# Kernel optimization log

Hardware: AMD Instinct MI355X
Metric: run time of the kernel (lower is better)

Reference implementation:

```python
import jax, jax.numpy as jnp
import numpy as np

D_HEAD = 64
MASK_FILL = -1000000.0


def setup_inputs() -> dict:
    key = jax.random.key(0)
    ks = jax.random.split(key, 5)
    batch, seq, d_model, n_heads, d_head = 4, 2048, 1024, 16, D_HEAD
    # xavier_uniform bound for [d_model, n_heads, d_head]: treated as fan_in=d_model, fan_out=n_heads*d_head
    bound_qkv = float(np.sqrt(6.0 / (d_model + n_heads * d_head)))
    bound_out = float(np.sqrt(6.0 / (d_head + n_heads * d_model)))
    return {
        "resid": jax.random.normal(ks[0], (batch, seq, d_model), dtype=jnp.float32),
        "W_Q": jax.random.uniform(ks[1], (d_model, n_heads, d_head), jnp.float32, -bound_qkv, bound_qkv),
        "W_K": jax.random.uniform(ks[2], (d_model, n_heads, d_head), jnp.float32, -bound_qkv, bound_qkv),
        "W_V": jax.random.uniform(ks[3], (d_model, n_heads, d_head), jnp.float32, -bound_qkv, bound_qkv),
        "W_out": jax.random.uniform(ks[4], (d_head, n_heads, d_model), jnp.float32, -bound_out, bound_out),
        "b_out": jnp.zeros((d_model,), dtype=jnp.float32),
    }


def reference(resid, W_Q, W_K, W_V, W_out, b_out):
    # resid: [b, s, d]; W_Q/K/V: [d, h, dh]; W_out: [dh, h, d]
    seq = resid.shape[1]
    d_head = W_Q.shape[-1]
    q = jnp.einsum('bsd,dhk->bshk', resid, W_Q)
    k = jnp.einsum('bsd,dhk->bshk', resid, W_K)
    v = jnp.einsum('bsd,dhk->bshk', resid, W_V)
    scores = jnp.einsum('bqhk,bkhd->bhqd', q, k.astype(q.dtype)) if False else jnp.einsum('bqhc,bshc->bhqs', q, k)
    scores = scores / jnp.sqrt(jnp.asarray(d_head, dtype=scores.dtype))
    causal_mask = jnp.triu(jnp.ones((seq, seq), dtype=bool), k=1)
    scores = jnp.where(causal_mask, MASK_FILL, scores)
    probs = jax.nn.softmax(scores, axis=-1)  # [b, h, q, s]
    z = jnp.einsum('bhqs,bshc->bqhc', probs, v)
    out = jnp.einsum('bqhc,chd->bqd', z, W_out) + b_out
    return out
```

## Files before the change

### kernel.cpp

```cpp
#include <hip/hip_runtime.h>
#include <hip/hip_bf16.h>


typedef short s16x8 __attribute__((ext_vector_type(8)));
typedef short s16x4 __attribute__((ext_vector_type(4)));
typedef float f32x4 __attribute__((ext_vector_type(4)));

#define MFMA_BF16(A, B, C) __builtin_amdgcn_mfma_f32_16x16x32_bf16((A), (B), (C), 0, 0, 0)

#if __has_builtin(__builtin_amdgcn_exp2f)
#define EXP2(x) __builtin_amdgcn_exp2f(x)
#else
#define EXP2(x) exp2f(x)
#endif
#if __has_builtin(__builtin_amdgcn_rcpf)
#define RCP(x) __builtin_amdgcn_rcpf(x)
#else
#define RCP(x) (1.0f / (x))
#endif

__device__ __forceinline__ short f2bf(float f) {
    __bf16 h = (__bf16)f;
    return __builtin_bit_cast(short, h);
}

__device__ __forceinline__ void gld16(const unsigned short* g, unsigned short* l) {
    __builtin_amdgcn_global_load_lds(
        (const __attribute__((address_space(1))) unsigned int*)g,
        (__attribute__((address_space(3))) unsigned int*)l, 16, 0, 0);
}

__global__ __launch_bounds__(256) void prep_fused(
    const float* __restrict__ resid, const float* __restrict__ WQ,
    const float* __restrict__ WK, const float* __restrict__ WV,
    const float* __restrict__ Wout,
    unsigned short* __restrict__ residb, unsigned short* __restrict__ Wqkvt,
    unsigned short* __restrict__ W2t)
{
    const int bid = blockIdx.x;
    if (bid < 8192) {
        const int i = bid * 256 + threadIdx.x;
        const float4 v = ((const float4*)resid)[i];
        s16x4 o;
        o[0] = f2bf(v.x); o[1] = f2bf(v.y); o[2] = f2bf(v.z); o[3] = f2bf(v.w);
        *(s16x4*)(residb + (size_t)i * 4) = o;
        return;
    }
    __shared__ unsigned short tile[64][66];
    const int id2 = bid - 8192;
    const int which = id2 >> 8;
    const int sub = id2 & 255;
    const int tx = threadIdx.x & 63, ty = threadIdx.x >> 6;
    if (which < 3) {
        const float* W = which == 0 ? WQ : (which == 1 ? WK : WV);
        unsigned short* Wt = Wqkvt + (size_t)which * 1024 * 1024;
        const int n0 = (sub & 15) * 64, k0 = (sub >> 4) * 64;
        #pragma unroll
        for (int i = ty; i < 64; i += 4)
            tile[i][tx] = (unsigned short)f2bf(W[(size_t)(k0 + i) * 1024 + n0 + tx]);
        __syncthreads();
        #pragma unroll
        for (int i = ty; i < 64; i += 4)
            Wt[(size_t)(n0 + i) * 1024 + k0 + tx] = tile[tx][i];
    } else {
        const int d0 = (sub & 15) * 64, h = sub >> 4;
        #pragma unroll
        for (int c = ty; c < 64; c += 4)
            tile[c][tx] = (unsigned short)f2bf(Wout[(size_t)(c * 16 + h) * 1024 + d0 + tx]);
        __syncthreads();
        #pragma unroll
        for (int i = ty; i < 64; i += 4)
            W2t[(size_t)(d0 + i) * 1024 + h * 64 + tx] = tile[tx][i];
    }
}

__global__ __launch_bounds__(512, 2) void gemm_qkv(
    const unsigned short* __restrict__ A,
    const unsigned short* __restrict__ Bt,
    unsigned short* __restrict__ Qb, unsigned short* __restrict__ Kb,
    unsigned short* __restrict__ Vt)
{
    extern __shared__ __align__(16) unsigned short S[];
    constexpr int LDK = 1024, NT = 16;
    const int tid = threadIdx.x, lane = tid & 63, w = tid >> 6;
    const int wm = w >> 2, wn = w & 3;
    const int quad = lane >> 4, fl = lane & 15;

    const int wg  = blockIdx.x;
    const int swz = (wg & 7) * 96 + (wg >> 3);
    const int bx  = swz % 12, by = swz / 12;
    const int m0  = by * 128, n0 = bx * 256;

    const int srow = tid >> 2;
    const int sk   = ((tid & 3) ^ ((tid >> 3) & 3)) * 8;
    const unsigned short* pa  = A  + (size_t)(m0 + srow) * LDK + sk;
    const unsigned short* pb0 = Bt + (size_t)(n0 + srow) * LDK + sk;
    const unsigned short* pb1 = Bt + (size_t)(n0 + 128 + srow) * LDK + sk;
    const int dst = tid * 8;

    const int sx   = (quad ^ ((fl >> 1) & 3)) * 8;
    const int arow = (wm * 64 + fl) * 32 + sx;
    const int brow = 8192 + (wn * 64 + fl) * 32 + sx;

    f32x4 acc[4][4];
    #pragma unroll
    for (int m = 0; m < 4; ++m)
        #pragma unroll
        for (int n = 0; n < 4; ++n) acc[m][n] = (f32x4){0.f, 0.f, 0.f, 0.f};

    gld16(pa,       S + dst);
    gld16(pb0,      S + 8192 + dst);
    gld16(pb1,      S + 12288 + dst);
    gld16(pa + 32,  S + 4096 + dst);
    gld16(pb0 + 32, S + 16384 + dst);
    gld16(pb1 + 32, S + 20480 + dst);
    gld16(pa + 64,  S + 24576 + dst);
    gld16(pb0 + 64, S + 24576 + 8192 + dst);
    gld16(pb1 + 64, S + 24576 + 12288 + dst);

    for (int t = 0; t < NT; ++t) {
        unsigned short* Sc = S + (t & 1) * 24576;
        unsigned short* Sn = S + ((t & 1) ^ 1) * 24576;

        if (t < NT - 1) asm volatile("s_waitcnt vmcnt(6)" ::: "memory");
        else            asm volatile("s_waitcnt vmcnt(3)" ::: "memory");
        __builtin_amdgcn_s_barrier();

        s16x8 af[4], bfr[4];
        #pragma unroll
        for (int mi = 0; mi < 4; ++mi) af[mi]  = *(const s16x8*)(Sc + arow + mi * 512);
        #pragma unroll
        for (int ni = 0; ni < 4; ++ni) bfr[ni] = *(const s16x8*)(Sc + brow + ni * 512);
        if (t < NT - 1) {
            const int ka = (t + 1) * 64 + 32;
            gld16(pa + ka,  Sn + 4096 + dst);
            gld16(pb0 + ka, Sn + 16384 + dst);
            gld16(pb1 + ka, Sn + 20480 + dst);
        }
        asm volatile("" ::: "memory");
        __builtin_amdgcn_s_barrier();
        __builtin_amdgcn_s_setprio(1);
        #pragma unroll
        for (int mi = 0; mi < 4; ++mi)
            #pragma unroll
            for (int ni = 0; ni < 4; ++ni)
                acc[mi][ni] = MFMA_BF16(af[mi], bfr[ni], acc[mi][ni]);
        __builtin_amdgcn_s_setprio(0);

        if (t < NT - 1) asm volatile("s_waitcnt vmcnt(6)" ::: "memory");
        else            asm volatile("s_waitcnt vmcnt(0)" ::: "memory");
        __builtin_amdgcn_s_barrier();
        #pragma unroll
        for (int mi = 0; mi < 4; ++mi) af[mi]  = *(const s16x8*)(Sc + 4096 + arow + mi * 512);
        #pragma unroll
        for (int ni = 0; ni < 4; ++ni) bfr[ni] = *(const s16x8*)(Sc + 8192 + brow + ni * 512);
        if (t < NT - 2) {
            const int ka = (t + 2) * 64;
            gld16(pa + ka,  Sc + dst);
            gld16(pb0 + ka, Sc + 8192 + dst);
            gld16(pb1 + ka, Sc + 12288 + dst);
        }
        asm volatile("" ::: "memory");
        __builtin_amdgcn_s_barrier();
        __builtin_amdgcn_s_setprio(1);
        #pragma unroll
        for (int mi = 0; mi < 4; ++mi)
            #pragma unroll
            for (int ni = 0; ni < 4; ++ni)
                acc[mi][ni] = MFMA_BF16(af[mi], bfr[ni], acc[mi][ni]);
        __builtin_amdgcn_s_setprio(0);
    }

    const int which = n0 >> 10;
    if (which < 2) {
        unsigned short* O = which == 0 ? Qb : Kb;
        const int cbase = (n0 & 1023) + wn * 64;
        #pragma unroll
        for (int mi = 0; mi < 4; ++mi) {
            const int row = m0 + wm * 64 + mi * 16 + quad * 4;
            #pragma unroll
            for (int ni = 0; ni < 4; ++ni) {
                const int col = cbase + ni * 16 + fl;
                #pragma unroll
                for (int r = 0; r < 4; ++r)
                    O[(size_t)(row + r) * 1024 + col] = (unsigned short)f2bf(acc[mi][ni][r]);
            }
        }
    } else {
        const int hh = ((n0 - 2048) >> 6) + wn;
        #pragma unroll
        for (int mi = 0; mi < 4; ++mi) {
            const int token = m0 + wm * 64 + mi * 16 + quad * 4;
            const int bb = token >> 11, ss = token & 2047;
            #pragma unroll
            for (int ni = 0; ni < 4; ++ni) {
                const int cl = ni * 16 + fl;
                s16x4 pv;
                pv[0] = f2bf(acc[mi][ni][0]); pv[1] = f2bf(acc[mi][ni][1]);
                pv[2] = f2bf(acc[mi][ni][2]); pv[3] = f2bf(acc[mi][ni][3]);
                *(s16x4*)(Vt + (size_t)((bb * 16 + hh) * 64 + cl) * 2048 + ss) = pv;
            }
        }
    }
}

template <int MODE>
__global__ __launch_bounds__(256, 2) void gemm_bt(
    const unsigned short* __restrict__ A,
    const unsigned short* __restrict__ Bt,
    float* __restrict__ Cf, const float* __restrict__ bias,
    int M, int N, int K)
{
    __shared__ __align__(16) unsigned short AB[2 * 128 * 72];
    const int tid  = threadIdx.x;
    const int lane = tid & 63;
    const int w    = tid >> 6;
    const int wm   = w & 1, wn = w >> 1;
    const int quad = lane >> 4, fl = lane & 15;
    const int m0 = blockIdx.y * 128, n0 = blockIdx.x * 128;

    const unsigned short* gp[9];
    unsigned ldso[9];
    #pragma unroll
    for (int i = 0; i < 9; ++i) {
        const int c = i * 256 + tid;
        const int cm = c % 1152;
        const int r = cm / 9, cl0 = cm % 9;
        const int cl = (cl0 == 8) ? 0 : cl0;
        gp[i] = (c < 1152 ? A + (size_t)(m0 + r) * K : Bt + (size_t)(n0 + r) * K) + cl * 8;
        ldso[i] = (unsigned)c * 8u;
    }

    f32x4 acc[4][4];
    #pragma unroll
    for (int i = 0; i < 4; ++i)
        #pragma unroll
        for (int j = 0; j < 4; ++j)
            acc[i][j] = (f32x4){0.f, 0.f, 0.f, 0.f};

    for (int kt = 0; kt < K; kt += 64) {
        __syncthreads();
        #pragma unroll
        for (int i = 0; i < 9; ++i)
            gld16(gp[i] + kt, AB + ldso[i]);
        __syncthreads();
        #pragma unroll
        for (int ko = 0; ko < 2; ++ko) {
            s16x8 af[4], bf[4];
            #pragma unroll
            for (int mi = 0; mi < 4; ++mi)
                af[mi] = *(const s16x8*)(AB + (wm * 64 + mi * 16 + fl) * 72 + ko * 32 + quad * 8);
            #pragma unroll
            for (int ni = 0; ni < 4; ++ni)
                bf[ni] = *(const s16x8*)(AB + 9216 + (wn * 64 + ni * 16 + fl) * 72 + ko * 32 + quad * 8);
            #pragma unroll
            for (int mi = 0; mi < 4; ++mi)
                #pragma unroll
                for (int ni = 0; ni < 4; ++ni)
                    acc[mi][ni] = MFMA_BF16(af[mi], bf[ni], acc[mi][ni]);
        }
    }

    #pragma unroll
    for (int ni = 0; ni < 4; ++ni) {
        const int col = n0 + wn * 64 + ni * 16 + fl;
        const float bv = bias[col];
        #pragma unroll
        for (int mi = 0; mi < 4; ++mi) {
            const int row = m0 + wm * 64 + mi * 16 + quad * 4;
            #pragma unroll
            for (int r = 0; r < 4; ++r)
                Cf[(size_t)(row + r) * N + col] = acc[mi][ni][r] + bv;
        }
    }
}

template <bool DIAG>
__device__ __forceinline__ void attn_tile(
    int s0, int wl, int wq0, int fl, int quad,
    const unsigned short* __restrict__ KV, const unsigned short* __restrict__ Vs,
    unsigned short* __restrict__ PbW,
    const s16x8 (&qfr)[2][2], f32x4 (&zt)[2][4], float (&ls)[2])
{
    const float SC = 0.18033688011112042f;
    const float M  = 32.0f;
    #pragma unroll
    for (int c4 = 0; c4 < 4; ++c4) {
        if (DIAG && c4 > wl) break;
        #pragma unroll
        for (int e = 0; e < 2; ++e) {
            const int f = 2 * c4 + e;
            const unsigned short* Krow = KV + (f * 16 + fl) * 72;
            const s16x8 kf0 = *(const s16x8*)(Krow + quad * 8);
            const s16x8 kf1 = *(const s16x8*)(Krow + 32 + quad * 8);
            #pragma unroll
            for (int g = 0; g < 2; ++g) {
                unsigned short* pw = PbW + (g * 16 + fl) * 36 + e * 16 + quad * 4;
                if (DIAG && f > 2 * wl + g) {
                    *(s16x4*)pw = (s16x4){0, 0, 0, 0};
                } else {
                    f32x4 z = (f32x4){0.f, 0.f, 0.f, 0.f};
                    z = MFMA_BF16(kf0, qfr[g][0], z);
                    z = MFMA_BF16(kf1, qfr[g][1], z);
                    float p[4];
                    #pragma unroll
                    for (int r = 0; r < 4; ++r) {
                        float arg = fmaf(z[r], SC, -M);
                        if (DIAG && f == 2 * wl + g) {
                            const int s = s0 + f * 16 + quad * 4 + r;
                            const int qi = wq0 + g * 16 + fl;
                            if (s > qi) arg = -100.f;
                        }
                        p[r] = EXP2(arg);
                    }
                    ls[g] += (p[0] + p[1]) + (p[2] + p[3]);
                    s16x4 pk;
                    pk[0] = f2bf(p[0]); pk[1] = f2bf(p[1]);
                    pk[2] = f2bf(p[2]); pk[3] = f2bf(p[3]);
                    *(s16x4*)pw = pk;
                }
            }
        }
        const s16x8 pf0 = *(const s16x8*)(PbW + fl * 36 + quad * 8);
        const s16x8 pf1 = *(const s16x8*)(PbW + (16 + fl) * 36 + quad * 8);
        #pragma unroll
        for (int mf = 0; mf < 4; ++mf) {
            const s16x8 vf = *(const s16x8*)(Vs + (mf * 16 + fl) * 136 + c4 * 32 + quad * 8);
            zt[0][mf] = MFMA_BF16(vf, pf0, zt[0][mf]);
            zt[1][mf] = MFMA_BF16(vf, pf1, zt[1][mf]);
        }
    }
}

__global__ __launch_bounds__(256, 3) void attn_causal(
    const unsigned short* __restrict__ Qb,
    const unsigned short* __restrict__ Kb,
    const unsigned short* __restrict__ Vt,
    unsigned short* __restrict__ Zb)
{
    __shared__ __align__(16) unsigned short KV[17920];
    __shared__ __align__(16) unsigned short Pb[4][32 * 36];
    const int tid = threadIdx.x, lane = tid & 63, w = tid >> 6;
    const int quad = lane >> 4, fl = lane & 15;
    const int lid = blockIdx.x;
    const int qb = 15 - (lid >> 6);
    const int bh = lid & 63, b = bh >> 4, h = bh & 15;
    const int wq0 = qb * 128 + w * 32;
    const int wl = w;

    const unsigned short* Kbase = Kb + (size_t)b * 2048 * 1024 + h * 64;
    const unsigned short* Vbase = Vt + (size_t)bh * 64 * 2048;
    unsigned short* PbW = Pb[w];
    const unsigned short* Vs = KV + 9216;

    s16x8 qfr[2][2];
    #pragma unroll
    for (int g = 0; g < 2; ++g) {
        const unsigned short* Qrow = Qb + (size_t)(b * 2048 + wq0 + g * 16 + fl) * 1024 + h * 64;
        qfr[g][0] = *(const s16x8*)(Qrow + quad * 8);
        qfr[g][1] = *(const s16x8*)(Qrow + 32 + quad * 8);
    }

    const unsigned short* gsp[9];
    int sadv[9];
    unsigned ldsb[9];
    #pragma unroll
    for (int i = 0; i < 9; ++i) {
        const int W = w + 4 * i;
        if (W < 35) {
            const int c = W * 64 + lane;
            if (c < 1152) {
                const int r = c / 9, cl0 = c % 9;
                const int cl = (cl0 == 8) ? 0 : cl0;
                gsp[i] = Kbase + r * 1024 + cl * 8;  sadv[i] = 128 * 1024;
            } else {
                const int cc = c - 1152;
                const int r = cc / 17, cl0 = cc % 17;
                const int cl = (cl0 == 16) ? 0 : cl0;
                gsp[i] = Vbase + r * 2048 + cl * 8;  sadv[i] = 128;
            }
            ldsb[i] = (unsigned)c * 8u;
        }
    }

    f32x4 zt[2][4];
    #pragma unroll
    for (int g = 0; g < 2; ++g)
        #pragma unroll
        for (int mf = 0; mf < 4; ++mf) zt[g][mf] = (f32x4){0.f, 0.f, 0.f, 0.f};
    float ls[2] = {0.f, 0.f};
    const int ntiles = qb + 1;

    for (int kt = 0; kt < ntiles; ++kt) {
        __syncthreads();
        #pragma unroll
        for (int i = 0; i < 9; ++i)
            if (w + 4 * i < 35)
                gld16(gsp[i], KV + ldsb[i]);
        #pragma unroll
        for (int i = 0; i < 9; ++i)
            if (w + 4 * i < 35)
                gsp[i] += sadv[i];
        __syncthreads();

        if (kt < qb) {
            attn_tile<false>(kt << 7, wl, wq0, fl, quad, KV, Vs, PbW, qfr, zt, ls);
        } else {
            attn_tile<true>(kt << 7, wl, wq0, fl, quad, KV, Vs, PbW, qfr, zt, ls);
        }
    }
    #pragma unroll
    for (int g = 0; g < 2; ++g) {
        float lt = ls[g];
        lt += __shfl_xor(lt, 16);
        lt += __shfl_xor(lt, 32);
        const float inv = RCP(lt);
        unsigned short* Zrow = Zb + (size_t)(b * 2048 + wq0 + g * 16 + fl) * 1024 + h * 64;
        #pragma unroll
        for (int mf = 0; mf < 4; ++mf) {
            s16x4 o;
            o[0] = f2bf(zt[g][mf][0] * inv); o[1] = f2bf(zt[g][mf][1] * inv);
            o[2] = f2bf(zt[g][mf][2] * inv); o[3] = f2bf(zt[g][mf][3] * inv);
            *(s16x4*)(Zrow + mf * 16 + quad * 4) = o;
        }
    }
}

extern "C" void kernel_launch(void* const* d_in, const int* in_sizes, int n_in,
                              void* d_out, int out_size, void* d_ws, size_t ws_size,
                              hipStream_t stream) {
    const float* resid = (const float*)d_in[0];
    const float* WQ    = (const float*)d_in[1];
    const float* WK    = (const float*)d_in[2];
    const float* WV    = (const float*)d_in[3];
    const float* Wout  = (const float*)d_in[4];
    const float* bout  = (const float*)d_in[5];
    float* out = (float*)d_out;

    char* p = (char*)d_ws;
    auto alloc = [&](size_t bytes) { void* r = (void*)p; p += (bytes + 255) & ~(size_t)255; return r; };
    unsigned short* residb = (unsigned short*)alloc(8192ull * 1024 * 2);
    unsigned short* Wqkvt  = (unsigned short*)alloc(3072ull * 1024 * 2);
    unsigned short* W2t    = (unsigned short*)alloc(1024ull * 1024 * 2);
    unsigned short* Qbuf   = (unsigned short*)alloc(8192ull * 1024 * 2);
    unsigned short* Kbuf   = (unsigned short*)alloc(8192ull * 1024 * 2);
    unsigned short* Vtb    = (unsigned short*)alloc(64ull * 64 * 2048 * 2);
    unsigned short* Zbuf   = (unsigned short*)alloc(8192ull * 1024 * 2);

    static bool s_attr = false;
    if (!s_attr) {
        hipFuncSetAttribute(reinterpret_cast<const void*>(gemm_qkv),
                            hipFuncAttributeMaxDynamicSharedMemorySize, 98304);
        s_attr = true;
    }

    prep_fused<<<9216, 256, 0, stream>>>(resid, WQ, WK, WV, Wout, residb, Wqkvt, W2t);
    gemm_qkv<<<768, 512, 98304, stream>>>(residb, Wqkvt, Qbuf, Kbuf, Vtb);
    attn_causal<<<1024, 256, 0, stream>>>(Qbuf, Kbuf, Vtb, Zbuf);
    gemm_bt<0><<<dim3(8, 64), 256, 0, stream>>>(Zbuf, W2t, out, bout, 8192, 1024, 1024);
}
```

Before: 265.4 us.

## Reuse deep-pipelined GEMM for output projection and compute softmax row sums via MFMA

New measurement: 250.2 us. -5.7%, faster.

```diff
diff --git a/kernel.cpp b/kernel.cpp
--- a/kernel.cpp
+++ b/kernel.cpp
@@ -74,21 +74,25 @@
     }
 }
 
-__global__ __launch_bounds__(512, 2) void gemm_qkv(
+template <int MODE>
+__global__ __launch_bounds__(512, 2) void gemm_deep(
     const unsigned short* __restrict__ A,
     const unsigned short* __restrict__ Bt,
     unsigned short* __restrict__ Qb, unsigned short* __restrict__ Kb,
-    unsigned short* __restrict__ Vt)
+    unsigned short* __restrict__ Vt,
+    float* __restrict__ Cf, const float* __restrict__ bias)
 {
     extern __shared__ __align__(16) unsigned short S[];
     constexpr int LDK = 1024, NT = 16;
+    constexpr int NBX = (MODE == 1) ? 12 : 4;
+    constexpr int XCH = (MODE == 1) ? 96 : 32;
     const int tid = threadIdx.x, lane = tid & 63, w = tid >> 6;
     const int wm = w >> 2, wn = w & 3;
     const int quad = lane >> 4, fl = lane & 15;
 
     const int wg  = blockIdx.x;
-    const int swz = (wg & 7) * 96 + (wg >> 3);
-    const int bx  = swz % 12, by = swz / 12;
+    const int swz = (wg & 7) * XCH + (wg >> 3);
+    const int bx  = swz % NBX, by = swz / NBX;
     const int m0  = by * 128, n0 = bx * 256;
 
     const int srow = tid >> 2;
@@ -171,106 +175,50 @@
         __builtin_amdgcn_s_setprio(0);
     }
 
-    const int which = n0 >> 10;
-    if (which < 2) {
-        unsigned short* O = which == 0 ? Qb : Kb;
-        const int cbase = (n0 & 1023) + wn * 64;
-        #pragma unroll
-        for (int mi = 0; mi < 4; ++mi) {
-            const int row = m0 + wm * 64 + mi * 16 + quad * 4;
-            #pragma unroll
-            for (int ni = 0; ni < 4; ++ni) {
-                const int col = cbase + ni * 16 + fl;
+    if (MODE == 0) {
+        #pragma unroll
+        for (int ni = 0; ni < 4; ++ni) {
+            const int col = n0 + wn * 64 + ni * 16 + fl;
+            const float bv = bias[col];
+            #pragma unroll
+            for (int mi = 0; mi < 4; ++mi) {
+                const int row = m0 + wm * 64 + mi * 16 + quad * 4;
                 #pragma unroll
                 for (int r = 0; r < 4; ++r)
-                    O[(size_t)(row + r) * 1024 + col] = (unsigned short)f2bf(acc[mi][ni][r]);
+                    Cf[(size_t)(row + r) * 1024 + col] = acc[mi][ni][r] + bv;
             }
         }
     } else {
-        const int hh = ((n0 - 2048) >> 6) + wn;
-        #pragma unroll
-        for (int mi = 0; mi < 4; ++mi) {
-            const int token = m0 + wm * 64 + mi * 16 + quad * 4;
-            const int bb = token >> 11, ss = token & 2047;
-            #pragma unroll
-            for (int ni = 0; ni < 4; ++ni) {
-                const int cl = ni * 16 + fl;
-                s16x4 pv;
-                pv[0] = f2bf(acc[mi][ni][0]); pv[1] = f2bf(acc[mi][ni][1]);
-                pv[2] = f2bf(acc[mi][ni][2]); pv[3] = f2bf(acc[mi][ni][3]);
-                *(s16x4*)(Vt + (size_t)((bb * 16 + hh) * 64 + cl) * 2048 + ss) = pv;
+        const int which = n0 >> 10;
+        if (which < 2) {
+            unsigned short* O = which == 0 ? Qb : Kb;
+            const int cbase = (n0 & 1023) + wn * 64;
+            #pragma unroll
+            for (int mi = 0; mi < 4; ++mi) {
+                const int row = m0 + wm * 64 + mi * 16 + quad * 4;
+                #pragma unroll
+                for (int ni = 0; ni < 4; ++ni) {
+                    const int col = cbase + ni * 16 + fl;
+                    #pragma unroll
+                    for (int r = 0; r < 4; ++r)
+                        O[(size_t)(row + r) * 1024 + col] = (unsigned short)f2bf(acc[mi][ni][r]);
+                }
             }
-        }
-    }
-}
-
-template <int MODE>
-__global__ __launch_bounds__(256, 2) void gemm_bt(
-    const unsigned short* __restrict__ A,
-    const unsigned short* __restrict__ Bt,
-    float* __restrict__ Cf, const float* __restrict__ bias,
-    int M, int N, int K)
-{
-    __shared__ __align__(16) unsigned short AB[2 * 128 * 72];
-    const int tid  = threadIdx.x;
-    const int lane = tid & 63;
-    const int w    = tid >> 6;
-    const int wm   = w & 1, wn = w >> 1;
-    const int quad = lane >> 4, fl = lane & 15;
-    const int m0 = blockIdx.y * 128, n0 = blockIdx.x * 128;
-
-    const unsigned short* gp[9];
-    unsigned ldso[9];
-    #pragma unroll
-    for (int i = 0; i < 9; ++i) {
-        const int c = i * 256 + tid;
-        const int cm = c % 1152;
-        const int r = cm / 9, cl0 = cm % 9;
-        const int cl = (cl0 == 8) ? 0 : cl0;
-        gp[i] = (c < 1152 ? A + (size_t)(m0 + r) * K : Bt + (size_t)(n0 + r) * K) + cl * 8;
-        ldso[i] = (unsigned)c * 8u;
-    }
-
-    f32x4 acc[4][4];
-    #pragma unroll
-    for (int i = 0; i < 4; ++i)
-        #pragma unroll
-        for (int j = 0; j < 4; ++j)
-            acc[i][j] = (f32x4){0.f, 0.f, 0.f, 0.f};
-
-    for (int kt = 0; kt < K; kt += 64) {
-        __syncthreads();
-        #pragma unroll
-        for (int i = 0; i < 9; ++i)
-            gld16(gp[i] + kt, AB + ldso[i]);
-        __syncthreads();
-        #pragma unroll
-        for (int ko = 0; ko < 2; ++ko) {
-            s16x8 af[4], bf[4];
-            #pragma unroll
-            for (int mi = 0; mi < 4; ++mi)
-                af[mi] = *(const s16x8*)(AB + (wm * 64 + mi * 16 + fl) * 72 + ko * 32 + quad * 8);
-            #pragma unroll
-            for (int ni = 0; ni < 4; ++ni)
-                bf[ni] = *(const s16x8*)(AB + 9216 + (wn * 64 + ni * 16 + fl) * 72 + ko * 32 + quad * 8);
-            #pragma unroll
-            for (int mi = 0; mi < 4; ++mi)
+        } else {
+            const int hh = ((n0 - 2048) >> 6) + wn;
+            #pragma unroll
+            for (int mi = 0; mi < 4; ++mi) {
+                const int token = m0 + wm * 64 + mi * 16 + quad * 4;
+                const int bb = token >> 11, ss = token & 2047;
                 #pragma unroll
-                for (int ni = 0; ni < 4; ++ni)
-                    acc[mi][ni] = MFMA_BF16(af[mi], bf[ni], acc[mi][ni]);
-        }
-    }
-
-    #pragma unroll
-    for (int ni = 0; ni < 4; ++ni) {
-        const int col = n0 + wn * 64 + ni * 16 + fl;
-        const float bv = bias[col];
-        #pragma unroll
-        for (int mi = 0; mi < 4; ++mi) {
-            const int row = m0 + wm * 64 + mi * 16 + quad * 4;
-            #pragma unroll
-            for (int r = 0; r < 4; ++r)
-                Cf[(size_t)(row + r) * N + col] = acc[mi][ni][r] + bv;
+                for (int ni = 0; ni < 4; ++ni) {
+                    const int cl = ni * 16 + fl;
+                    s16x4 pv;
+                    pv[0] = f2bf(acc[mi][ni][0]); pv[1] = f2bf(acc[mi][ni][1]);
+                    pv[2] = f2bf(acc[mi][ni][2]); pv[3] = f2bf(acc[mi][ni][3]);
+                    *(s16x4*)(Vt + (size_t)((bb * 16 + hh) * 64 + cl) * 2048 + ss) = pv;
+                }
+            }
         }
     }
 }
@@ -280,10 +228,11 @@
     int s0, int wl, int wq0, int fl, int quad,
     const unsigned short* __restrict__ KV, const unsigned short* __restrict__ Vs,
     unsigned short* __restrict__ PbW,
-    const s16x8 (&qfr)[2][2], f32x4 (&zt)[2][4], float (&ls)[2])
+    const s16x8 (&qfr)[2][2], f32x4 (&zt)[2][4], f32x4 (&lsa)[2])
 {
     const float SC = 0.18033688011112042f;
     const float M  = 32.0f;
+    const s16x8 ones = {16256, 16256, 16256, 16256, 16256, 16256, 16256, 16256};
     #pragma unroll
     for (int c4 = 0; c4 < 4; ++c4) {
         if (DIAG && c4 > wl) break;
@@ -313,7 +262,6 @@
                         }
                         p[r] = EXP2(arg);
                     }
-                    ls[g] += (p[0] + p[1]) + (p[2] + p[3]);
                     s16x4 pk;
                     pk[0] = f2bf(p[0]); pk[1] = f2bf(p[1]);
                     pk[2] = f2bf(p[2]); pk[3] = f2bf(p[3]);
@@ -323,12 +271,16 @@
         }
         const s16x8 pf0 = *(const s16x8*)(PbW + fl * 36 + quad * 8);
         const s16x8 pf1 = *(const s16x8*)(PbW + (16 + fl) * 36 + quad * 8);
+        __builtin_amdgcn_s_setprio(1);
+        lsa[0] = MFMA_BF16(ones, pf0, lsa[0]);
+        lsa[1] = MFMA_BF16(ones, pf1, lsa[1]);
         #pragma unroll
         for (int mf = 0; mf < 4; ++mf) {
             const s16x8 vf = *(const s16x8*)(Vs + (mf * 16 + fl) * 136 + c4 * 32 + quad * 8);
             zt[0][mf] = MFMA_BF16(vf, pf0, zt[0][mf]);
             zt[1][mf] = MFMA_BF16(vf, pf1, zt[1][mf]);
         }
+        __builtin_amdgcn_s_setprio(0);
     }
 }
 
@@ -388,7 +340,7 @@
     for (int g = 0; g < 2; ++g)
         #pragma unroll
         for (int mf = 0; mf < 4; ++mf) zt[g][mf] = (f32x4){0.f, 0.f, 0.f, 0.f};
-    float ls[2] = {0.f, 0.f};
+    f32x4 lsa[2] = {(f32x4){0.f, 0.f, 0.f, 0.f}, (f32x4){0.f, 0.f, 0.f, 0.f}};
     const int ntiles = qb + 1;
 
     for (int kt = 0; kt < ntiles; ++kt) {
@@ -404,17 +356,14 @@
         __syncthreads();
 
         if (kt < qb) {
-            attn_tile<false>(kt << 7, wl, wq0, fl, quad, KV, Vs, PbW, qfr, zt, ls);
+            attn_tile<false>(kt << 7, wl, wq0, fl, quad, KV, Vs, PbW, qfr, zt, lsa);
         } else {
-            attn_tile<true>(kt << 7, wl, wq0, fl, quad, KV, Vs, PbW, qfr, zt, ls);
+            attn_tile<true>(kt << 7, wl, wq0, fl, quad, KV, Vs, PbW, qfr, zt, lsa);
         }
     }
     #pragma unroll
     for (int g = 0; g < 2; ++g) {
-        float lt = ls[g];
-        lt += __shfl_xor(lt, 16);
-        lt += __shfl_xor(lt, 32);
-        const float inv = RCP(lt);
+        const float inv = RCP(lsa[g][0]);
         unsigned short* Zrow = Zb + (size_t)(b * 2048 + wq0 + g * 16 + fl) * 1024 + h * 64;
         #pragma unroll
         for (int mf = 0; mf < 4; ++mf) {
@@ -449,13 +398,17 @@
 
     static bool s_attr = false;
     if (!s_attr) {
-        hipFuncSetAttribute(reinterpret_cast<const void*>(gemm_qkv),
+        hipFuncSetAttribute(reinterpret_cast<const void*>(gemm_deep<1>),
+                            hipFuncAttributeMaxDynamicSharedMemorySize, 98304);
+        hipFuncSetAttribute(reinterpret_cast<const void*>(gemm_deep<0>),
                             hipFuncAttributeMaxDynamicSharedMemorySize, 98304);
         s_attr = true;
     }
 
     prep_fused<<<9216, 256, 0, stream>>>(resid, WQ, WK, WV, Wout, residb, Wqkvt, W2t);
-    gemm_qkv<<<768, 512, 98304, stream>>>(residb, Wqkvt, Qbuf, Kbuf, Vtb);
+    gemm_deep<1><<<768, 512, 98304, stream>>>(residb, Wqkvt, Qbuf, Kbuf, Vtb,
+                                              nullptr, nullptr);
     attn_causal<<<1024, 256, 0, stream>>>(Qbuf, Kbuf, Vtb, Zbuf);
-    gemm_bt<0><<<dim3(8, 64), 256, 0, stream>>>(Zbuf, W2t, out, bout, 8192, 1024, 1024);
-}
+    gemm_deep<0><<<256, 512, 98304, stream>>>(Zbuf, W2t, nullptr, nullptr, nullptr,
+                                              out, bout);
+}
```
